# Kernel optimization log

Hardware: AMD Instinct MI355X
Metric: run time of the kernel (lower is better)

Reference implementation:

```python
import jax, jax.numpy as jnp
import numpy as np

B, C, H, W = 8, 80, 128, 128
K = 100
MAX_OBJS = 128
N_GT = 256  # 32 GT boxes per image
HM_W, WH_W, OFF_W = 1.0, 0.1, 1.0
BETA = 0.1  # iou_map weight ('Ct IoU Loss x 0.1')


def setup_inputs() -> dict:
    key = jax.random.key(0)
    ks = jax.random.split(key, 12)
    hm = jax.random.normal(ks[0], (B, C, H, W), jnp.float32)
    wh = jax.random.normal(ks[1], (B, 2, H, W), jnp.float32) * 2.0 + 8.0
    reg = jax.random.normal(ks[2], (B, 2, H, W), jnp.float32) * 0.1
    hm_target = jax.random.uniform(ks[3], (B, C, H, W), jnp.float32) * 0.99
    wh_target = jax.random.uniform(ks[4], (B, MAX_OBJS, 2), jnp.float32) * 20.0 + 2.0
    reg_target = jax.random.uniform(ks[5], (B, MAX_OBJS, 2), jnp.float32)
    reg_mask = jax.random.randint(ks[6], (B, MAX_OBJS), 0, 2).astype(jnp.int32)
    ind = jax.random.randint(ks[7], (B, MAX_OBJS), 0, H * W).astype(jnp.int32)
    cx = jax.random.uniform(ks[8], (N_GT,)) * (W - 1)
    cy = jax.random.uniform(ks[9], (N_GT,)) * (H - 1)
    bw = jax.random.uniform(ks[10], (N_GT,)) * 30.0 + 2.0
    bh = jax.random.uniform(ks[11], (N_GT,)) * 30.0 + 2.0
    target_box = jnp.stack([cx - bw / 2, cy - bh / 2, cx + bw / 2, cy + bh / 2], -1).astype(jnp.float32)
    target_bidx = jnp.repeat(jnp.arange(B), N_GT // B).astype(jnp.int32)
    return {"hm": hm, "wh": wh, "reg": reg, "hm_target": hm_target,
            "wh_target": wh_target, "reg_target": reg_target,
            "reg_mask": reg_mask, "ind": ind,
            "target_box": target_box, "target_bidx": target_bidx}


def _gather_feat(feat, ind):
    # feat [B, ch, H, W], ind [B, M] spatial indices -> [B, M, ch]
    b, ch = feat.shape[0], feat.shape[1]
    f = feat.reshape(b, ch, -1).transpose(0, 2, 1)  # [B, HW, ch]
    return jnp.take_along_axis(f, ind[:, :, None], axis=1)


def _pairwise_iou(boxes1, boxes2):
    # boxes1 [K,4], boxes2 [N,4], xyxy -> [K,N]
    a1 = jnp.maximum(boxes1[:, 2] - boxes1[:, 0], 0.0) * jnp.maximum(boxes1[:, 3] - boxes1[:, 1], 0.0)
    a2 = jnp.maximum(boxes2[:, 2] - boxes2[:, 0], 0.0) * jnp.maximum(boxes2[:, 3] - boxes2[:, 1], 0.0)
    lt = jnp.maximum(boxes1[:, None, :2], boxes2[None, :, :2])
    rb = jnp.minimum(boxes1[:, None, 2:], boxes2[None, :, 2:])
    whi = jnp.clip(rb - lt, 0.0)
    inter = whi[..., 0] * whi[..., 1]
    union = a1[:, None] + a2[None, :] - inter
    return inter / jnp.maximum(union, 1e-7)


def _decode(hm_s, wh, reg):
    # _nms: 3x3 max-pool peak keeping
    hmax = jax.lax.reduce_window(hm_s, -jnp.inf, jax.lax.max,
                                 (1, 1, 3, 3), (1, 1, 1, 1),
                                 [(0, 0), (0, 0), (1, 1), (1, 1)])
    hm_k = jnp.where(hmax == hm_s, hm_s, 0.0)
    # global top-K over C*H*W (equivalent to per-class topK then topK-of-topK)
    scores, inds = jax.lax.top_k(hm_k.reshape(B, -1), K)
    clses = inds // (H * W)
    sinds = inds % (H * W)
    ys_i = sinds // W
    xs_i = sinds % W
    r = _gather_feat(reg, sinds)  # [B,K,2] sub-pixel offsets
    xs = xs_i.astype(jnp.float32) + r[..., 0]
    ys = ys_i.astype(jnp.float32) + r[..., 1]
    w = _gather_feat(wh, sinds)   # [B,K,2]
    boxes = jnp.stack([xs - w[..., 0] / 2, ys - w[..., 1] / 2,
                       xs + w[..., 0] / 2, ys + w[..., 1] / 2], -1)
    return boxes, scores, clses, ys_i, xs_i


def _focal_loss(pred, gt):
    # CenterNet focal loss; pred already sigmoid+clamped
    pos = gt == 1.0
    neg_w = (1.0 - gt) ** 4
    pos_loss = jnp.sum(jnp.where(pos, jnp.log(pred) * (1.0 - pred) ** 2, 0.0))
    neg_loss = jnp.sum(jnp.where(pos, 0.0, jnp.log(1.0 - pred) * pred ** 2 * neg_w))
    num_pos = jnp.sum(pos.astype(jnp.float32))
    return jnp.where(num_pos > 0, -(pos_loss + neg_loss) / jnp.maximum(num_pos, 1.0), -neg_loss)


def _reg_l1(out, mask, ind, tgt):
    pred = _gather_feat(out, ind)                       # [B, M, 2]
    m = jnp.broadcast_to(mask.astype(jnp.float32)[:, :, None], pred.shape)
    return jnp.sum(jnp.abs(pred * m - tgt * m)) / (jnp.sum(m) + 1e-4)


def reference(hm, wh, reg, hm_target, wh_target, reg_target, reg_mask, ind, target_box, target_bidx):
    hm_s = jnp.clip(jax.nn.sigmoid(hm), 1e-4, 1.0 - 1e-4)  # _sigmoid
    boxes, scores, clses, ys_i, xs_i = _decode(hm_s, wh, reg)
    # per-image pairwise IoU vs GT boxes of the same image, max over GT
    iou_all = jax.vmap(lambda bx: _pairwise_iou(bx, target_box))(boxes)  # [B,K,N]
    bmask = target_bidx[None, None, :] == jnp.arange(B)[:, None, None]
    iou = jnp.max(jnp.where(bmask, iou_all, 0.0), axis=-1)              # [B,K]
    # scatter IoU into dense heatmap-shaped iou_map at (b, cls, y, x)
    b_idx = jnp.broadcast_to(jnp.arange(B)[:, None], (B, K))
    iou_map = jnp.zeros_like(hm_s).at[b_idx, clses, ys_i, xs_i].set(iou)
    hm_t = jnp.clip(hm_target + BETA * iou_map, 0.0, 1.0)
    hm_loss = _focal_loss(hm_s, hm_t)
    wh_loss = _reg_l1(wh, reg_mask, ind, wh_target)
    off_loss = _reg_l1(reg, reg_mask, ind, reg_target)
    loss = HM_W * hm_loss + WH_W * wh_loss + OFF_W * off_loss
    return loss, hm_loss, wh_loss, off_loss
```

## Files before the change

kernel.cpp:

```cpp
#include <hip/hip_runtime.h>
#include <math.h>

#define B_ 8
#define C_ 80
#define H_ 128
#define W_ 128
#define K_ 100
#define MAXOBJS_ 128
#define NGT_ 256
#define HW_ (H_*W_)
#define CHW_ (C_*H_*W_)
#define TOT_ (B_*CHW_)
#define NBINS_ 4096
#define BCAP_ 4096
#define DCAP_ 128
#define CAPLDS_ 1280
#define DLOC_ 128
#define BLOC_ 768
#define HCHUNK_ 32
#define NEGINF_ (-INFINITY)

#define OFF_MISC    64
#define OFF_LISTCNT 96
#define OFF_SELDONE 160
#define OFF_THRB    192
#define OFF_CNTA    224
#define OFF_CNTB    256
#define OFF_ACCP    512
#define OFF_HIST    1024
#define ZERO_ALL    132096
#define OFF_DEFV    132096
#define OFF_DEFI    136192
#define OFF_BORV    140288
#define OFF_BORI    271360
#define OFF_LIST    402432
#define CAP_REQ     196608ull
#define CAP_MAX     262144ull

__device__ __forceinline__ unsigned skey(float x){
    unsigned u = __float_as_uint(x);
    return (u & 0x80000000u) ? ~u : (u | 0x80000000u);
}

__device__ __forceinline__ void find_thr(const unsigned* __restrict__ lh,
                                         unsigned* __restrict__ part,
                                         unsigned target,
                                         unsigned* out_thr, unsigned* out_cum){
    int t = threadIdx.x;
    unsigned s = 0;
    #pragma unroll
    for(int k=0;k<16;++k) s += lh[t*16+k];
    part[t] = s;
    __syncthreads();
    for(int off=1; off<256; off<<=1){
        unsigned v = (t+off<256) ? part[t+off] : 0u;
        __syncthreads();
        part[t] += v;
        __syncthreads();
    }
    unsigned nxt = (t<255) ? part[t+1] : 0u;
    if(part[t] >= target && nxt < target){
        unsigned cum = nxt;
        int thr = t*16;
        for(int bin=t*16+15; bin>=t*16; --bin){
            unsigned c = lh[bin];
            if(cum + c >= target){ thr = bin; break; }
            cum += c;
        }
        *out_thr = (unsigned)thr;
        *out_cum = cum;
    }
    __syncthreads();
}

struct Row { float v[4]; float le, re; };

__device__ __forceinline__ Row loadrow(const float* __restrict__ P, int y, int xq){
    Row r;
    if(y < 0 || y >= H_){
        r.v[0]=r.v[1]=r.v[2]=r.v[3]=r.le=r.re=NEGINF_;
        return r;
    }
    const float4 f = *(const float4*)(P + y*W_ + xq*4);
    r.v[0]=f.x; r.v[1]=f.y; r.v[2]=f.z; r.v[3]=f.w;
    r.le = (xq==0) ? NEGINF_ : P[y*W_ + xq*4 - 1];
    r.re = (xq==31)? NEGINF_ : P[y*W_ + xq*4 + 4];
    return r;
}

__device__ __forceinline__ void hmax4(const Row& r, float h[4]){
    h[0]=fmaxf(fmaxf(r.le,  r.v[0]), r.v[1]);
    h[1]=fmaxf(fmaxf(r.v[0],r.v[1]), r.v[2]);
    h[2]=fmaxf(fmaxf(r.v[1],r.v[2]), r.v[3]);
    h[3]=fmaxf(fmaxf(r.v[2],r.v[3]), r.re);
}

__global__ __launch_bounds__(256) void k_main(const float* __restrict__ hm,
        const float* __restrict__ hmt, double* __restrict__ accp,
        unsigned* __restrict__ listcnt, float* __restrict__ vlist,
        int* __restrict__ ilist, int capB){
    __shared__ int2 lbuf[CAPLDS_];
    __shared__ float wsum[4];
    __shared__ unsigned lcnt, lbase;
    int t = threadIdx.x;
    int plane = blockIdx.x >> 1;
    int half  = blockIdx.x & 1;
    int b = plane / C_;
    int cls = plane - b*C_;
    const float* P = hm  + (size_t)plane*HW_;
    const float* T = hmt + (size_t)plane*HW_;
    int idx0 = cls*HW_;

    if(t==0) lcnt=0u;
    __syncthreads();

    int xq = t & 31;
    int y0 = half*64 + (t>>5)*8;
    Row rp = loadrow(P, y0-1, xq);
    Row rc = loadrow(P, y0,   xq);
    float hp[4]; hmax4(rp, hp);
    float acc = 0.f;
    for(int rr=0; rr<8; ++rr){
        int y = y0 + rr;
        Row rn = loadrow(P, y+1, xq);
        float hn[4]; hmax4(rn, hn);
        float vv[4] = {rc.v[0], rc.v[1], rc.v[2], rc.v[3]};
        float lrv[4];
        lrv[0]=fmaxf(rc.le,  vv[1]);
        lrv[1]=fmaxf(vv[0],  vv[2]);
        lrv[2]=fmaxf(vv[1],  vv[3]);
        lrv[3]=fmaxf(vv[2],  rc.re);
        float4 tg = *(const float4*)(T + y*W_ + xq*4);
        float tgv[4] = {tg.x, tg.y, tg.z, tg.w};
        #pragma unroll
        for(int j=0;j<4;++j){
            float v = vv[j];
            bool pk = (v>=lrv[j]) && (v>=hp[j]) && (v>=hn[j]);
            if(pk && capB){
                unsigned p = atomicAdd(&lcnt, 1u);
                int2 e; e.x = __float_as_int(v); e.y = idx0 + y*W_ + xq*4 + j;
                if(p < CAPLDS_) lbuf[p] = e;
                else {
                    unsigned g = atomicAdd(&listcnt[b], 1u);
                    if(g < (unsigned)capB){
                        vlist[(size_t)b*capB + g] = v;
                        ilist[(size_t)b*capB + g] = e.y;
                    }
                }
            }
            float pr = 1.f/(1.f + __expf(-v));
            pr = fminf(fmaxf(pr, 1e-4f), 1.f - 1e-4f);
            float q = 1.f - tgv[j]; float q2 = q*q;
            acc += __logf(1.f - pr) * pr * pr * q2 * q2;
        }
        #pragma unroll
        for(int j=0;j<4;++j) hp[j] = fmaxf(lrv[j], vv[j]);
        rc = rn;
    }
    __syncthreads();

    unsigned n = lcnt; if(n > CAPLDS_) n = CAPLDS_;
    if(capB && t==0) lbase = atomicAdd(&listcnt[b], n);
    #pragma unroll
    for(int off=32; off>0; off>>=1) acc += __shfl_xor(acc, off, 64);
    if((t & 63) == 0) wsum[t>>6] = acc;
    __syncthreads();
    if(capB){
        for(unsigned i=t;i<n;i+=256){
            unsigned g = lbase + i;
            if(g < (unsigned)capB){
                vlist[(size_t)b*capB + g] = __int_as_float(lbuf[i].x);
                ilist[(size_t)b*capB + g] = lbuf[i].y;
            }
        }
    }
    if(t==0) atomicAdd(&accp[blockIdx.x & 63], (double)(wsum[0]+wsum[1]+wsum[2]+wsum[3]));
}

__global__ __launch_bounds__(256) void k_hist(const float* __restrict__ vlist,
        const unsigned* __restrict__ listcnt, int capB,
        unsigned* __restrict__ hist){
    __shared__ unsigned lh[2][NBINS_];
    int b = blockIdx.x / HCHUNK_;
    int chunk = blockIdx.x - b*HCHUNK_;
    int t = threadIdx.x;
    unsigned* lhw = lh[t>>7];
    for(int i=t;i<2*NBINS_;i+=256) (&lh[0][0])[i]=0u;
    __syncthreads();
    unsigned n = listcnt[b]; if(n > (unsigned)capB) n = (unsigned)capB;
    const float* V = vlist + (size_t)b*capB;
    for(unsigned i = chunk*256u + t; i < n; i += HCHUNK_*256u){
        atomicAdd(&lhw[skey(V[i])>>20], 1u);
    }
    __syncthreads();
    for(int i=t;i<NBINS_;i+=256){
        unsigned c = lh[0][i] + lh[1][i];
        if(c) atomicAdd(&hist[b*NBINS_+i], c);
    }
}

__global__ void k_thresh(const unsigned* __restrict__ hist, unsigned* __restrict__ thrbin){
    __shared__ unsigned lh[NBINS_];
    __shared__ unsigned part[256];
    __shared__ unsigned thrs, cums;
    int b = blockIdx.x, t = threadIdx.x;
    for(int i=t;i<NBINS_;i+=256) lh[i]=hist[b*NBINS_+i];
    if(t==0){ thrs=0u; cums=0u; }
    __syncthreads();
    find_thr(lh, part, (unsigned)K_, &thrs, &cums);
    if(t==0) thrbin[b]=thrs;
}

__global__ __launch_bounds__(256) void k_scan(const float* __restrict__ vlist,
        const int* __restrict__ ilist,
        const unsigned* __restrict__ listcnt, int capB,
        const unsigned* __restrict__ thrbin,
        unsigned* __restrict__ cntA, unsigned* __restrict__ cntB,
        float* __restrict__ defv, int* __restrict__ defi,
        float* __restrict__ borv, int* __restrict__ bori){
    __shared__ int2 dloc[DLOC_];
    __shared__ int2 bloc[BLOC_];
    __shared__ unsigned dc, bc, dbase, bbase;
    int b = blockIdx.x >> 6;
    int chunk = blockIdx.x & 63;
    int t = threadIdx.x;
    if(t==0){ dc=0u; bc=0u; }
    __syncthreads();
    unsigned thr = thrbin[b];
    unsigned n = listcnt[b]; if(n > (unsigned)capB) n = (unsigned)capB;
    const float* V = vlist + (size_t)b*capB;
    const int*   I = ilist + (size_t)b*capB;
    for(unsigned i = chunk*256u + t; i < n; i += 64u*256u){
        float v = V[i];
        unsigned bin = skey(v) >> 20;
        if(bin > thr){
            int2 e; e.x = __float_as_int(v); e.y = I[i];
            unsigned p = atomicAdd(&dc, 1u);
            if(p < DLOC_) dloc[p] = e;
            else { unsigned g = atomicAdd(&cntA[b],1u); if(g<DCAP_){ defv[b*DCAP_+g]=v; defi[b*DCAP_+g]=e.y; } }
        } else if(bin == thr){
            int2 e; e.x = __float_as_int(v); e.y = I[i];
            unsigned p = atomicAdd(&bc, 1u);
            if(p < BLOC_) bloc[p] = e;
            else { unsigned g = atomicAdd(&cntB[b],1u); if(g<BCAP_){ borv[b*BCAP_+g]=v; bori[b*BCAP_+g]=e.y; } }
        }
    }
    __syncthreads();
    unsigned dn = dc < DLOC_ ? dc : DLOC_;
    unsigned bn = bc < BLOC_ ? bc : BLOC_;
    if(t==0){
        dbase = dn ? atomicAdd(&cntA[b], dn) : 0u;
        bbase = bn ? atomicAdd(&cntB[b], bn) : 0u;
    }
    __syncthreads();
    for(unsigned i=t;i<dn;i+=256){
        unsigned g = dbase + i;
        if(g < DCAP_){ defv[b*DCAP_+g]=__int_as_float(dloc[i].x); defi[b*DCAP_+g]=dloc[i].y; }
    }
    for(unsigned i=t;i<bn;i+=256){
        unsigned g = bbase + i;
        if(g < BCAP_){ borv[b*BCAP_+g]=__int_as_float(bloc[i].x); bori[b*BCAP_+g]=bloc[i].y; }
    }
}

__device__ __forceinline__ bool is_peak_scalar(const float* __restrict__ hm, int idx, float v){
    int w = idx & (W_-1);
    int h = (idx >> 7) & (H_-1);
    bool peak = true;
    #pragma unroll
    for(int dy=-1; dy<=1; ++dy){
        int hh = h + dy;
        if(hh < 0 || hh >= H_) continue;
        #pragma unroll
        for(int dx=-1; dx<=1; ++dx){
            if(dy==0 && dx==0) continue;
            int ww = w + dx;
            if(ww < 0 || ww >= W_) continue;
            peak = peak && (v >= __ldg(&hm[idx + dy*W_ + dx]));
        }
    }
    return peak;
}

__global__ __launch_bounds__(256) void k_peaks_fb(const float* __restrict__ hm,
        unsigned* __restrict__ hist){
    __shared__ unsigned lh[NBINS_];
    int t = threadIdx.x;
    int b = blockIdx.x >> 8;
    int blk = blockIdx.x & 255;
    int base = b*CHW_ + blk*(CHW_/256);
    for(int i=t;i<NBINS_;i+=256) lh[i]=0u;
    __syncthreads();
    for(int it=0; it<CHW_/256/256; ++it){
        int idx = base + it*256 + t;
        float v = hm[idx];
        if(is_peak_scalar(hm, idx, v)) atomicAdd(&lh[skey(v)>>20], 1u);
    }
    __syncthreads();
    for(int i=t;i<NBINS_;i+=256){ unsigned c=lh[i]; if(c) atomicAdd(&hist[b*NBINS_+i], c); }
}

__global__ __launch_bounds__(256) void k_collect(const float* __restrict__ hm,
        const unsigned* __restrict__ thrbin,
        unsigned* __restrict__ cntA, unsigned* __restrict__ cntB,
        float* __restrict__ defv, int* __restrict__ defi,
        float* __restrict__ borv, int* __restrict__ bori){
    int idx = blockIdx.x*256 + threadIdx.x;
    float v = hm[idx];
    if(!is_peak_scalar(hm, idx, v)) return;
    int b = idx / CHW_;
    unsigned bin = skey(v) >> 20;
    unsigned thr = thrbin[b];
    if(bin > thr){
        unsigned p = atomicAdd(&cntA[b], 1u);
        if(p < DCAP_){ defv[b*DCAP_+p] = v; defi[b*DCAP_+p] = idx - b*CHW_; }
    } else if(bin == thr){
        unsigned p = atomicAdd(&cntB[b], 1u);
        if(p < BCAP_){ borv[b*BCAP_+p] = v; bori[b*BCAP_+p] = idx - b*CHW_; }
    }
}

__global__ __launch_bounds__(256) void k_select(const float* __restrict__ hm,
        const float* __restrict__ hmt, const float* __restrict__ wh,
        const float* __restrict__ reg, const float* __restrict__ tbox,
        const int* __restrict__ tbid,
        const float* __restrict__ wht, const float* __restrict__ regt,
        const int* __restrict__ mask, const int* __restrict__ ind,
        const unsigned* __restrict__ cntA, const unsigned* __restrict__ cntB,
        const float* __restrict__ defv, const int* __restrict__ defi,
        const float* __restrict__ borv, const int* __restrict__ bori,
        double* __restrict__ accum, const double* __restrict__ accp,
        int* __restrict__ misc, unsigned* __restrict__ seldone,
        float* __restrict__ out){
    int b = blockIdx.x, t = threadIdx.x;
    __shared__ float gbox[NGT_][4];
    __shared__ float garea[NGT_];
    __shared__ float sv[BCAP_];
    __shared__ int   si[BCAP_];
    __shared__ unsigned h2[NBINS_];
    __shared__ unsigned t4[BCAP_];
    __shared__ unsigned part[256];
    __shared__ int  rvI[256];
    __shared__ int  sel[K_];
    __shared__ float sbx[K_][4];
    __shared__ float sa[K_];
    __shared__ int   ioui[K_];
    __shared__ float r0s[256], r1s[256], r2s[256];
    __shared__ double dpos[256], dneg[256];
    __shared__ int    inp[256];
    __shared__ double dsum[64];
    __shared__ unsigned gcnt, selc, t3c, t4c;
    __shared__ unsigned thr2s, cum2s, thr3s, need3s;
    __shared__ int wsel, amlast;

    int nA = (int)cntA[b]; if(nA>DCAP_) nA=DCAP_; if(nA>K_) nA=K_;
    int nB = (int)cntB[b]; if(nB>BCAP_) nB=BCAP_;
    int m = K_ - nA; if(m>nB) m=nB; if(m<0) m=0;

    if(t==0){ gcnt=0u; selc=(unsigned)nA; t3c=0u; t4c=0u;
              thr2s=0u; cum2s=0u; thr3s=0u; need3s=0u; }
    for(int i=t;i<NBINS_;i+=256) h2[i]=0u;
    __syncthreads();

    for(int i=t;i<NGT_;i+=256){
        if(tbid[i]==b){
            unsigned p = atomicAdd(&gcnt, 1u);
            float gx1=tbox[i*4+0], gy1=tbox[i*4+1], gx2=tbox[i*4+2], gy2=tbox[i*4+3];
            gbox[p][0]=gx1; gbox[p][1]=gy1; gbox[p][2]=gx2; gbox[p][3]=gy2;
            garea[p]=fmaxf(gx2-gx1,0.f)*fmaxf(gy2-gy1,0.f);
        }
    }
    for(int i=t;i<nB;i+=256){ sv[i]=borv[b*BCAP_+i]; si[i]=bori[b*BCAP_+i]; }
    for(int i=t;i<nA;i+=256) sel[i]=defi[b*DCAP_+i];
    __syncthreads();

    if(m>0){
        for(int i=t;i<nB;i+=256) atomicAdd(&h2[(skey(sv[i])>>8)&0xFFFu], 1u);
        __syncthreads();
        find_thr(h2, part, (unsigned)m, &thr2s, &cum2s);
        unsigned thr2 = thr2s, need2 = (unsigned)m - cum2s;
        for(int i=t;i<nB;i+=256){
            unsigned sb=(skey(sv[i])>>8)&0xFFFu;
            if(sb>thr2){ unsigned p=atomicAdd(&selc,1u); if(p<K_) sel[p]=si[i]; }
            else if(sb==thr2){ unsigned p=atomicAdd(&t3c,1u); if(p<BCAP_) t4[p]=(unsigned)i; }
        }
        __syncthreads();
        unsigned nt3=t3c; if(nt3>BCAP_) nt3=BCAP_;
        part[t]=0u;
        __syncthreads();
        for(unsigned i=t;i<nt3;i+=256) atomicAdd(&part[skey(sv[t4[i]])&0xFFu], 1u);
        __syncthreads();
        for(int off=1; off<256; off<<=1){
            unsigned v = (t+off<256)? part[t+off] : 0u;
            __syncthreads();
            part[t] += v;
            __syncthreads();
        }
        {
            unsigned nxt = (t<255)? part[t+1] : 0u;
            if(part[t] >= need2 && nxt < need2){ thr3s=(unsigned)t; need3s=need2-nxt; }
        }
        __syncthreads();
        unsigned thr3=thr3s, need3=need3s;
        for(unsigned i=t;i<nt3;i+=256){
            unsigned ci=t4[i];
            unsigned lb=skey(sv[ci])&0xFFu;
            if(lb>thr3){ unsigned p=atomicAdd(&selc,1u); if(p<K_) sel[p]=si[ci]; }
            else if(lb==thr3){ unsigned p=atomicAdd(&t4c,1u); if(p<NBINS_) h2[p]=(unsigned)si[ci]; }
        }
        __syncthreads();
        unsigned n4=t4c; if(n4>NBINS_) n4=NBINS_;
        if(need3 >= n4){
            for(unsigned i=t;i<n4;i+=256){ unsigned p=atomicAdd(&selc,1u); if(p<K_) sel[p]=(int)h2[i]; }
            __syncthreads();
        } else {
            for(unsigned it=0; it<need3; ++it){
                int bi=0x7FFFFFFF;
                for(unsigned i=t;i<n4;i+=256){ int w=(int)h2[i]; bi = (w<bi)?w:bi; }
                rvI[t]=bi;
                __syncthreads();
                for(int st=128;st>0;st>>=1){
                    if(t<st){ int w=rvI[t+st]; if(w<rvI[t]) rvI[t]=w; }
                    __syncthreads();
                }
                if(t==0){ wsel=rvI[0]; unsigned p=selc; selc=p+1u; if(p<K_) sel[p]=wsel; }
                __syncthreads();
                int w=wsel;
                for(unsigned i=t;i<n4;i+=256) if((int)h2[i]==w) h2[i]=0x7FFFFFFFu;
                __syncthreads();
            }
        }
    }
    __syncthreads();

    int nsel=(int)selc; if(nsel>K_) nsel=K_;
    for(int k=t;k<nsel;k+=256){
        int idx = sel[k];
        int cls = idx / HW_;
        int sp  = idx - cls*HW_;
        int yi = sp>>7, xi = sp&(W_-1);
        float rr0 = reg[(b*2+0)*HW_+sp], rr1 = reg[(b*2+1)*HW_+sp];
        float w0 = wh[(b*2+0)*HW_+sp],  w1 = wh[(b*2+1)*HW_+sp];
        float xs = (float)xi + rr0, ys = (float)yi + rr1;
        float x1=xs-w0*0.5f, y1=ys-w1*0.5f, x2=xs+w0*0.5f, y2=ys+w1*0.5f;
        sbx[k][0]=x1; sbx[k][1]=y1; sbx[k][2]=x2; sbx[k][3]=y2;
        sa[k] = fmaxf(x2-x1,0.f)*fmaxf(y2-y1,0.f);
        ioui[k] = 0;
    }
    __syncthreads();
    int ng = (int)gcnt; if(ng>NGT_) ng=NGT_;
    for(int pi=t; pi<nsel*ng; pi+=256){
        int k = pi / ng, g = pi - k*ng;
        float x1=sbx[k][0], y1=sbx[k][1], x2=sbx[k][2], y2=sbx[k][3];
        float ix1=fmaxf(x1,gbox[g][0]), iy1=fmaxf(y1,gbox[g][1]);
        float ix2=fminf(x2,gbox[g][2]), iy2=fminf(y2,gbox[g][3]);
        float iw=fmaxf(ix2-ix1,0.f), ih=fmaxf(iy2-iy1,0.f);
        float inter=iw*ih;
        float uni = sa[k] + garea[g] - inter;
        float iou = inter / fmaxf(uni, 1e-7f);
        atomicMax(&ioui[k], __float_as_int(iou));
    }
    __syncthreads();
    double myPos = 0.0, myNeg = 0.0; int myNp = 0;
    for(int k=t;k<nsel;k+=256){
        float best = __int_as_float(ioui[k]);
        int gidx = b*CHW_ + sel[k];
        float v = hm[gidx];
        float p = 1.f/(1.f + __expf(-v));
        p = fminf(fmaxf(p, 1e-4f), 1.f - 1e-4f);
        float gt0 = hmt[gidx];
        float q0 = 1.f - gt0; float q02 = q0*q0;
        float neg0 = __logf(1.f - p) * p * p * q02 * q02;
        float gt1 = fminf(gt0 + 0.1f*best, 1.f);
        if(gt1 == 1.f){
            myNp += 1;
            float op = 1.f - p;
            myPos += (double)(__logf(p)*op*op);
            myNeg += (double)(-neg0);
        } else {
            float q1 = 1.f - gt1; float q12 = q1*q1;
            float neg1 = __logf(1.f - p) * p * p * q12 * q12;
            myNeg += (double)(neg1 - neg0);
        }
    }
    dpos[t]=myPos; dneg[t]=myNeg; inp[t]=myNp;
    __syncthreads();
    for(int st=128; st>0; st>>=1){
        if(t<st){ dpos[t]+=dpos[t+st]; dneg[t]+=dneg[t+st]; inp[t]+=inp[t+st]; }
        __syncthreads();
    }
    if(t==0){
        if(dpos[0]!=0.0) atomicAdd(&accum[1], dpos[0]);
        if(dneg[0]!=0.0) atomicAdd(&accum[2], dneg[0]);
        if(inp[0])       atomicAdd(&misc[0], inp[0]);
    }

    __threadfence();
    __syncthreads();
    if(t==0){
        unsigned d = atomicAdd(seldone, 1u);
        amlast = (d == (unsigned)(B_-1));
    }
    __syncthreads();
    if(amlast){
        __threadfence();
        float whn=0.f, offn=0.f, ms=0.f;
        for(int i=t;i<B_*MAXOBJS_;i+=256){
            int bb = i >> 7;
            float mk = (float)mask[i];
            int id = ind[i];
            float p0 = wh[(bb*2+0)*HW_+id], p1 = wh[(bb*2+1)*HW_+id];
            whn += mk*(fabsf(p0 - wht[2*i]) + fabsf(p1 - wht[2*i+1]));
            float q0 = reg[(bb*2+0)*HW_+id], q1 = reg[(bb*2+1)*HW_+id];
            offn += mk*(fabsf(q0 - regt[2*i]) + fabsf(q1 - regt[2*i+1]));
            ms += 2.f*mk;
        }
        r0s[t]=whn; r1s[t]=offn; r2s[t]=ms;
        if(t < 64) dsum[t] = __hip_atomic_load(&accp[t], __ATOMIC_RELAXED, __HIP_MEMORY_SCOPE_AGENT);
        __syncthreads();
        for(int st=128; st>0; st>>=1){
            if(t<st){ r0s[t]+=r0s[t+st]; r1s[t]+=r1s[t+st]; r2s[t]+=r2s[t+st]; }
            __syncthreads();
        }
        if(t==0){
            double nb = 0.0;
            for(int i=0;i<64;++i) nb += dsum[i];
            double pos = __hip_atomic_load(&accum[1], __ATOMIC_RELAXED, __HIP_MEMORY_SCOPE_AGENT);
            double nd  = __hip_atomic_load(&accum[2], __ATOMIC_RELAXED, __HIP_MEMORY_SCOPE_AGENT);
            int np = __hip_atomic_load(&misc[0], __ATOMIC_RELAXED, __HIP_MEMORY_SCOPE_AGENT);
            double neg = nb + nd;
            float hm_loss = (np > 0) ? (float)(-(pos + neg)/(double)np) : (float)(-neg);
            float msum = r2s[0];
            float wh_loss  = r0s[0] / (msum + 1e-4f);
            float off_loss = r1s[0] / (msum + 1e-4f);
            out[0] = hm_loss + 0.1f*wh_loss + off_loss;
            out[1] = hm_loss; out[2] = wh_loss; out[3] = off_loss;
        }
    }
}

extern "C" void kernel_launch(void* const* d_in, const int* in_sizes, int n_in,
                              void* d_out, int out_size, void* d_ws, size_t ws_size,
                              hipStream_t stream){
    const float* hm   = (const float*)d_in[0];
    const float* wh   = (const float*)d_in[1];
    const float* reg  = (const float*)d_in[2];
    const float* hmt  = (const float*)d_in[3];
    const float* wht  = (const float*)d_in[4];
    const float* regt = (const float*)d_in[5];
    const int*   mask = (const int*)d_in[6];
    const int*   ind  = (const int*)d_in[7];
    const float* tbox = (const float*)d_in[8];
    const int*   tbid = (const int*)d_in[9];

    char* ws = (char*)d_ws;
    double*   accum   = (double*)ws;
    int*      misc    = (int*)(ws + OFF_MISC);
    unsigned* listcnt = (unsigned*)(ws + OFF_LISTCNT);
    unsigned* seldone = (unsigned*)(ws + OFF_SELDONE);
    unsigned* thrbin  = (unsigned*)(ws + OFF_THRB);
    unsigned* cntA    = (unsigned*)(ws + OFF_CNTA);
    unsigned* cntB    = (unsigned*)(ws + OFF_CNTB);
    double*   accp    = (double*)(ws + OFF_ACCP);
    unsigned* hist    = (unsigned*)(ws + OFF_HIST);
    float*    defv    = (float*)(ws + OFF_DEFV);
    int*      defi    = (int*)(ws + OFF_DEFI);
    float*    borv    = (float*)(ws + OFF_BORV);
    int*      bori    = (int*)(ws + OFF_BORI);

    size_t capB = 0;
    if(ws_size >= (size_t)OFF_LIST + CAP_REQ*(size_t)B_*8ull){
        capB = (ws_size - (size_t)OFF_LIST) / ((size_t)B_*8ull);
        if(capB > CAP_MAX) capB = CAP_MAX;
        capB &= ~3ull;
    }
    float* vlist = (float*)(ws + OFF_LIST);
    int*   ilist = (int*)(ws + OFF_LIST + (size_t)B_*capB*4ull);

    hipMemsetAsync(ws, 0, ZERO_ALL, stream);
    if(capB){
        k_main<<<B_*C_*2, 256, 0, stream>>>(hm, hmt, accp, listcnt, vlist, ilist, (int)capB);
        k_hist<<<B_*HCHUNK_, 256, 0, stream>>>(vlist, listcnt, (int)capB, hist);
        k_thresh<<<B_, 256, 0, stream>>>(hist, thrbin);
        k_scan<<<B_*64, 256, 0, stream>>>(vlist, ilist, listcnt, (int)capB, thrbin,
                                          cntA, cntB, defv, defi, borv, bori);
    } else {
        k_main<<<B_*C_*2, 256, 0, stream>>>(hm, hmt, accp, listcnt, vlist, ilist, 0);
        k_peaks_fb<<<B_*256, 256, 0, stream>>>(hm, hist);
        k_thresh<<<B_, 256, 0, stream>>>(hist, thrbin);
        k_collect<<<TOT_/256, 256, 0, stream>>>(hm, thrbin, cntA, cntB,
                                                defv, defi, borv, bori);
    }
    k_select<<<B_, 256, 0, stream>>>(hm, hmt, wh, reg, tbox, tbid,
                                     wht, regt, mask, ind, cntA, cntB,
                                     defv, defi, borv, bori, accum, accp, misc,
                                     seldone, (float*)d_out);
    (void)in_sizes; (void)n_in; (void)out_size;
}
```

Before: 83.72 us.

## Split monolithic select kernel into top-k, IoU, and final-loss kernels

The single per-image select kernel is split into three launches. A top-k kernel writes the selected indices to workspace, an IoU/focal-correction kernel reads them back, and a one-block kernel computes the regression losses and the final outputs. This removes the last-block-done atomic counter and lowers per-kernel shared memory, which may improve occupancy and scheduling. In exchange it adds two kernel launches and a global round trip for the selected indices.

```diff
diff --git a/kernel.cpp b/kernel.cpp
--- a/kernel.cpp
+++ b/kernel.cpp
@@ -22,7 +22,7 @@
 
 #define OFF_MISC    64
 #define OFF_LISTCNT 96
-#define OFF_SELDONE 160
+#define OFF_NSEL    288
 #define OFF_THRB    192
 #define OFF_CNTA    224
 #define OFF_CNTB    256
@@ -33,7 +33,8 @@
 #define OFF_DEFI    136192
 #define OFF_BORV    140288
 #define OFF_BORI    271360
-#define OFF_LIST    402432
+#define OFF_SELIDX  402432
+#define OFF_LIST    406528
 #define CAP_REQ     196608ull
 #define CAP_MAX     262144ull
 
@@ -320,21 +321,12 @@
     }
 }
 
-__global__ __launch_bounds__(256) void k_select(const float* __restrict__ hm,
-        const float* __restrict__ hmt, const float* __restrict__ wh,
-        const float* __restrict__ reg, const float* __restrict__ tbox,
-        const int* __restrict__ tbid,
-        const float* __restrict__ wht, const float* __restrict__ regt,
-        const int* __restrict__ mask, const int* __restrict__ ind,
+__global__ __launch_bounds__(256) void k_topk(
         const unsigned* __restrict__ cntA, const unsigned* __restrict__ cntB,
         const float* __restrict__ defv, const int* __restrict__ defi,
         const float* __restrict__ borv, const int* __restrict__ bori,
-        double* __restrict__ accum, const double* __restrict__ accp,
-        int* __restrict__ misc, unsigned* __restrict__ seldone,
-        float* __restrict__ out){
+        int* __restrict__ selbuf, unsigned* __restrict__ nselbuf){
     int b = blockIdx.x, t = threadIdx.x;
-    __shared__ float gbox[NGT_][4];
-    __shared__ float garea[NGT_];
     __shared__ float sv[BCAP_];
     __shared__ int   si[BCAP_];
     __shared__ unsigned h2[NBINS_];
@@ -342,34 +334,17 @@
     __shared__ unsigned part[256];
     __shared__ int  rvI[256];
     __shared__ int  sel[K_];
-    __shared__ float sbx[K_][4];
-    __shared__ float sa[K_];
-    __shared__ int   ioui[K_];
-    __shared__ float r0s[256], r1s[256], r2s[256];
-    __shared__ double dpos[256], dneg[256];
-    __shared__ int    inp[256];
-    __shared__ double dsum[64];
-    __shared__ unsigned gcnt, selc, t3c, t4c;
+    __shared__ unsigned selc, t3c, t4c;
     __shared__ unsigned thr2s, cum2s, thr3s, need3s;
-    __shared__ int wsel, amlast;
+    __shared__ int wsel;
 
     int nA = (int)cntA[b]; if(nA>DCAP_) nA=DCAP_; if(nA>K_) nA=K_;
     int nB = (int)cntB[b]; if(nB>BCAP_) nB=BCAP_;
     int m = K_ - nA; if(m>nB) m=nB; if(m<0) m=0;
 
-    if(t==0){ gcnt=0u; selc=(unsigned)nA; t3c=0u; t4c=0u;
+    if(t==0){ selc=(unsigned)nA; t3c=0u; t4c=0u;
               thr2s=0u; cum2s=0u; thr3s=0u; need3s=0u; }
     for(int i=t;i<NBINS_;i+=256) h2[i]=0u;
-    __syncthreads();
-
-    for(int i=t;i<NGT_;i+=256){
-        if(tbid[i]==b){
-            unsigned p = atomicAdd(&gcnt, 1u);
-            float gx1=tbox[i*4+0], gy1=tbox[i*4+1], gx2=tbox[i*4+2], gy2=tbox[i*4+3];
-            gbox[p][0]=gx1; gbox[p][1]=gy1; gbox[p][2]=gx2; gbox[p][3]=gy2;
-            garea[p]=fmaxf(gx2-gx1,0.f)*fmaxf(gy2-gy1,0.f);
-        }
-    }
     for(int i=t;i<nB;i+=256){ sv[i]=borv[b*BCAP_+i]; si[i]=bori[b*BCAP_+i]; }
     for(int i=t;i<nA;i+=256) sel[i]=defi[b*DCAP_+i];
     __syncthreads();
@@ -432,8 +407,42 @@
         }
     }
     __syncthreads();
-
     int nsel=(int)selc; if(nsel>K_) nsel=K_;
+    for(int i=t;i<nsel;i+=256) selbuf[b*MAXOBJS_+i] = sel[i];
+    if(t==0) nselbuf[b] = (unsigned)nsel;
+}
+
+__global__ __launch_bounds__(256) void k_iou(const float* __restrict__ hm,
+        const float* __restrict__ hmt, const float* __restrict__ wh,
+        const float* __restrict__ reg, const float* __restrict__ tbox,
+        const int* __restrict__ tbid,
+        const int* __restrict__ selbuf, const unsigned* __restrict__ nselbuf,
+        double* __restrict__ accum, int* __restrict__ misc){
+    int b = blockIdx.x, t = threadIdx.x;
+    __shared__ float gbox[NGT_][4];
+    __shared__ float garea[NGT_];
+    __shared__ int   sel[K_];
+    __shared__ float sbx[K_][4];
+    __shared__ float sa[K_];
+    __shared__ int   ioui[K_];
+    __shared__ double dpos[256], dneg[256];
+    __shared__ int    inp[256];
+    __shared__ unsigned gcnt;
+
+    if(t==0) gcnt=0u;
+    __syncthreads();
+    int nsel = (int)nselbuf[b]; if(nsel>K_) nsel=K_;
+    for(int i=t;i<NGT_;i+=256){
+        if(tbid[i]==b){
+            unsigned p = atomicAdd(&gcnt, 1u);
+            float gx1=tbox[i*4+0], gy1=tbox[i*4+1], gx2=tbox[i*4+2], gy2=tbox[i*4+3];
+            gbox[p][0]=gx1; gbox[p][1]=gy1; gbox[p][2]=gx2; gbox[p][3]=gy2;
+            garea[p]=fmaxf(gx2-gx1,0.f)*fmaxf(gy2-gy1,0.f);
+        }
+    }
+    for(int i=t;i<nsel;i+=256) sel[i]=selbuf[b*MAXOBJS_+i];
+    __syncthreads();
+
     for(int k=t;k<nsel;k+=256){
         int idx = sel[k];
         int cls = idx / HW_;
@@ -494,48 +503,48 @@
         if(dneg[0]!=0.0) atomicAdd(&accum[2], dneg[0]);
         if(inp[0])       atomicAdd(&misc[0], inp[0]);
     }
-
-    __threadfence();
-    __syncthreads();
+}
+
+__global__ __launch_bounds__(256) void k_heads(const float* __restrict__ wh,
+        const float* __restrict__ reg, const float* __restrict__ wht,
+        const float* __restrict__ regt, const int* __restrict__ mask,
+        const int* __restrict__ ind, const double* __restrict__ accum,
+        const double* __restrict__ accp, const int* __restrict__ misc,
+        float* __restrict__ out){
+    int t = threadIdx.x;
+    __shared__ float r0s[256], r1s[256], r2s[256];
+    __shared__ double dsum[64];
+    float whn=0.f, offn=0.f, ms=0.f;
+    for(int i=t;i<B_*MAXOBJS_;i+=256){
+        int bb = i >> 7;
+        float mk = (float)mask[i];
+        int id = ind[i];
+        float p0 = wh[(bb*2+0)*HW_+id], p1 = wh[(bb*2+1)*HW_+id];
+        whn += mk*(fabsf(p0 - wht[2*i]) + fabsf(p1 - wht[2*i+1]));
+        float q0 = reg[(bb*2+0)*HW_+id], q1 = reg[(bb*2+1)*HW_+id];
+        offn += mk*(fabsf(q0 - regt[2*i]) + fabsf(q1 - regt[2*i+1]));
+        ms += 2.f*mk;
+    }
+    r0s[t]=whn; r1s[t]=offn; r2s[t]=ms;
+    if(t < 64) dsum[t] = __hip_atomic_load(&accp[t], __ATOMIC_RELAXED, __HIP_MEMORY_SCOPE_AGENT);
+    __syncthreads();
+    for(int st=128; st>0; st>>=1){
+        if(t<st){ r0s[t]+=r0s[t+st]; r1s[t]+=r1s[t+st]; r2s[t]+=r2s[t+st]; }
+        __syncthreads();
+    }
     if(t==0){
-        unsigned d = atomicAdd(seldone, 1u);
-        amlast = (d == (unsigned)(B_-1));
-    }
-    __syncthreads();
-    if(amlast){
-        __threadfence();
-        float whn=0.f, offn=0.f, ms=0.f;
-        for(int i=t;i<B_*MAXOBJS_;i+=256){
-            int bb = i >> 7;
-            float mk = (float)mask[i];
-            int id = ind[i];
-            float p0 = wh[(bb*2+0)*HW_+id], p1 = wh[(bb*2+1)*HW_+id];
-            whn += mk*(fabsf(p0 - wht[2*i]) + fabsf(p1 - wht[2*i+1]));
-            float q0 = reg[(bb*2+0)*HW_+id], q1 = reg[(bb*2+1)*HW_+id];
-            offn += mk*(fabsf(q0 - regt[2*i]) + fabsf(q1 - regt[2*i+1]));
-            ms += 2.f*mk;
-        }
-        r0s[t]=whn; r1s[t]=offn; r2s[t]=ms;
-        if(t < 64) dsum[t] = __hip_atomic_load(&accp[t], __ATOMIC_RELAXED, __HIP_MEMORY_SCOPE_AGENT);
-        __syncthreads();
-        for(int st=128; st>0; st>>=1){
-            if(t<st){ r0s[t]+=r0s[t+st]; r1s[t]+=r1s[t+st]; r2s[t]+=r2s[t+st]; }
-            __syncthreads();
-        }
-        if(t==0){
-            double nb = 0.0;
-            for(int i=0;i<64;++i) nb += dsum[i];
-            double pos = __hip_atomic_load(&accum[1], __ATOMIC_RELAXED, __HIP_MEMORY_SCOPE_AGENT);
-            double nd  = __hip_atomic_load(&accum[2], __ATOMIC_RELAXED, __HIP_MEMORY_SCOPE_AGENT);
-            int np = __hip_atomic_load(&misc[0], __ATOMIC_RELAXED, __HIP_MEMORY_SCOPE_AGENT);
-            double neg = nb + nd;
-            float hm_loss = (np > 0) ? (float)(-(pos + neg)/(double)np) : (float)(-neg);
-            float msum = r2s[0];
-            float wh_loss  = r0s[0] / (msum + 1e-4f);
-            float off_loss = r1s[0] / (msum + 1e-4f);
-            out[0] = hm_loss + 0.1f*wh_loss + off_loss;
-            out[1] = hm_loss; out[2] = wh_loss; out[3] = off_loss;
-        }
+        double nb = 0.0;
+        for(int i=0;i<64;++i) nb += dsum[i];
+        double pos = __hip_atomic_load(&accum[1], __ATOMIC_RELAXED, __HIP_MEMORY_SCOPE_AGENT);
+        double nd  = __hip_atomic_load(&accum[2], __ATOMIC_RELAXED, __HIP_MEMORY_SCOPE_AGENT);
+        int np = __hip_atomic_load(&misc[0], __ATOMIC_RELAXED, __HIP_MEMORY_SCOPE_AGENT);
+        double neg = nb + nd;
+        float hm_loss = (np > 0) ? (float)(-(pos + neg)/(double)np) : (float)(-neg);
+        float msum = r2s[0];
+        float wh_loss  = r0s[0] / (msum + 1e-4f);
+        float off_loss = r1s[0] / (msum + 1e-4f);
+        out[0] = hm_loss + 0.1f*wh_loss + off_loss;
+        out[1] = hm_loss; out[2] = wh_loss; out[3] = off_loss;
     }
 }
 
@@ -557,7 +566,7 @@
     double*   accum   = (double*)ws;
     int*      misc    = (int*)(ws + OFF_MISC);
     unsigned* listcnt = (unsigned*)(ws + OFF_LISTCNT);
-    unsigned* seldone = (unsigned*)(ws + OFF_SELDONE);
+    unsigned* nselbuf = (unsigned*)(ws + OFF_NSEL);
     unsigned* thrbin  = (unsigned*)(ws + OFF_THRB);
     unsigned* cntA    = (unsigned*)(ws + OFF_CNTA);
     unsigned* cntB    = (unsigned*)(ws + OFF_CNTB);
@@ -567,6 +576,7 @@
     int*      defi    = (int*)(ws + OFF_DEFI);
     float*    borv    = (float*)(ws + OFF_BORV);
     int*      bori    = (int*)(ws + OFF_BORI);
+    int*      selbuf  = (int*)(ws + OFF_SELIDX);
 
     size_t capB = 0;
     if(ws_size >= (size_t)OFF_LIST + CAP_REQ*(size_t)B_*8ull){
@@ -591,9 +601,11 @@
         k_collect<<<TOT_/256, 256, 0, stream>>>(hm, thrbin, cntA, cntB,
                                                 defv, defi, borv, bori);
     }
-    k_select<<<B_, 256, 0, stream>>>(hm, hmt, wh, reg, tbox, tbid,
-                                     wht, regt, mask, ind, cntA, cntB,
-                                     defv, defi, borv, bori, accum, accp, misc,
-                                     seldone, (float*)d_out);
+    k_topk<<<B_, 256, 0, stream>>>(cntA, cntB, defv, defi, borv, bori,
+                                   selbuf, nselbuf);
+    k_iou<<<B_, 256, 0, stream>>>(hm, hmt, wh, reg, tbox, tbid,
+                                  selbuf, nselbuf, accum, misc);
+    k_heads<<<1, 256, 0, stream>>>(wh, reg, wht, regt, mask, ind,
+                                   accum, accp, misc, (float*)d_out);
     (void)in_sizes; (void)n_in; (void)out_size;
 }
```

Result: no change. 85.02 us (+1.6%).
